# Performance work log

Measured on AMD Instinct MI355X. Metric: run time of the kernel, lower is better.

The kernel has to match this reference:

```python
import jax, jax.numpy as jnp
import numpy as np

FRACTION_BITS = 16
INTEGER_BITS = 16


def round_to_fixed(x):
    # floor-quantize to 2^-16 steps, clamp to signed 16-bit integer range
    delta = 2.0 ** (-FRACTION_BITS)
    bound = 2.0 ** (INTEGER_BITS - 1)
    return jnp.clip(jnp.floor(x / delta) * delta, -bound, bound - 1.0)


def setup_inputs() -> dict:
    key = jax.random.key(0)
    k1, k2, k3, k4 = jax.random.split(key, 4)
    N, IN_F, OUT_F = 4096, 4096, 4096
    inp = jax.random.normal(k1, (N, IN_F), dtype=jnp.float32)
    # reset_parameters: shift ~ U(-10,-1), sign ~ U(-1,0), bias ~ U(-b,b), b=1/sqrt(fan_in)
    shift = jax.random.uniform(k2, (OUT_F, IN_F), minval=-10.0, maxval=-1.0, dtype=jnp.float32)
    sign = jax.random.uniform(k3, (OUT_F, IN_F), minval=-1.0, maxval=0.0, dtype=jnp.float32)
    b = 1.0 / np.sqrt(IN_F)
    bias = jax.random.uniform(k4, (OUT_F,), minval=-b, maxval=b, dtype=jnp.float32)
    return {"input": inp, "shift": shift, "sign": sign, "bias": bias}


def reference(input, shift, sign, bias):
    # eager (non-kernel) path of LinearShiftFunction.forward
    q_in = round_to_fixed(input)
    q_bias = round_to_fixed(bias)
    s = jnp.clip(sign, -1.0, 1.0)
    v = jnp.exp2(jnp.round(shift)) * jnp.sign(s)  # [out_f, in_f] power-of-two weights
    out = q_in @ v.T + q_bias[None, :]
    return out
```

## Files before the change

### kernel.cpp

```cpp
#include <hip/hip_runtime.h>
#include <hip/hip_bf16.h>


#define BM 256
#define BN 256
#define BK 64

typedef __bf16 bf16_t;
typedef __attribute__((ext_vector_type(8))) __bf16 bf16x8;
typedef __attribute__((ext_vector_type(4))) __bf16 bf16x4;
typedef __attribute__((ext_vector_type(4))) float f32x4;

__device__ __forceinline__ float q16(float x) {
    float f = floorf(x * 65536.0f) * (1.0f / 65536.0f);
    return fminf(fmaxf(f, -32768.0f), 32767.0f);
}

__global__ void convert_kernel(const float* __restrict__ in,
                               const float* __restrict__ shift,
                               const float* __restrict__ sign_,
                               bf16_t* __restrict__ aq,
                               bf16_t* __restrict__ wq, int nvec) {
    int stride = gridDim.x * blockDim.x;
    for (int i = blockIdx.x * blockDim.x + threadIdx.x; i < nvec; i += stride) {
        float4 v = reinterpret_cast<const float4*>(in)[i];
        bf16x4 oa;
        oa[0] = (bf16_t)q16(v.x);
        oa[1] = (bf16_t)q16(v.y);
        oa[2] = (bf16_t)q16(v.z);
        oa[3] = (bf16_t)q16(v.w);
        reinterpret_cast<bf16x4*>(aq)[i] = oa;

        float4 sh = reinterpret_cast<const float4*>(shift)[i];
        float4 sg = reinterpret_cast<const float4*>(sign_)[i];
        float shs[4] = {sh.x, sh.y, sh.z, sh.w};
        float sgs[4] = {sg.x, sg.y, sg.z, sg.w};
        bf16x4 ow;
#pragma unroll
        for (int j = 0; j < 4; ++j) {
            float s = fminf(fmaxf(sgs[j], -1.0f), 1.0f);
            float sv = (s > 0.0f) ? 1.0f : ((s < 0.0f) ? -1.0f : 0.0f);
            ow[j] = (bf16_t)(exp2f(rintf(shs[j])) * sv);
        }
        reinterpret_cast<bf16x4*>(wq)[i] = ow;
    }
}


#define VMW(N) asm volatile("s_waitcnt vmcnt(" #N ")" ::: "memory")
#define BARF() do { __builtin_amdgcn_s_barrier(); asm volatile("" ::: "memory"); } while (0)

#define STAGE(LDSOFF, SRC) do {                                                          \
    const bf16_t* _s = (SRC);                                                            \
    bf16_t* _d = &lds[(LDSOFF)] + tid * 8;                                               \
    __builtin_amdgcn_global_load_lds((const __attribute__((address_space(1))) void*)_s,  \
                                     (__attribute__((address_space(3))) void*)_d,        \
                                     16, 0, 0);                                          \
    __builtin_amdgcn_global_load_lds(                                                    \
        (const __attribute__((address_space(1))) void*)(_s + (size_t)64 * K),            \
        (__attribute__((address_space(3))) void*)(_d + 4096), 16, 0, 0);                 \
} while (0)

#define READ_A(BUF, MH) do {                                                             \
    const bf16_t* _As = &lds[(BUF) * 32768 + wm * 8192];                                 \
    _Pragma("unroll") for (int m = 0; m < 4; ++m)                                        \
        _Pragma("unroll") for (int kk = 0; kk < 2; ++kk)                                 \
            af[m][kk] = *(const bf16x8*)&_As[((MH) * 64 + m * 16 + fr) * 64 +            \
                                             ((((kk << 2) | hi) ^ fr7) << 3)];           \
} while (0)

#define READ_B(BUF, NH, BF) do {                                                         \
    const bf16_t* _Bs = &lds[(BUF) * 32768 + 16384 + (wn >> 1) * 8192];                  \
    _Pragma("unroll") for (int n = 0; n < 2; ++n)                                        \
        _Pragma("unroll") for (int kk = 0; kk < 2; ++kk)                                 \
            BF[n][kk] = *(const bf16x8*)&_Bs[((wn & 1) * 64 + ((NH) * 2 + n) * 16 + fr)  \
                                                 * 64 +                                  \
                                             ((((kk << 2) | hi) ^ fr7) << 3)];           \
} while (0)

#define QUAD(MH, NH, BF) do {                                                            \
    _Pragma("unroll") for (int m = 0; m < 4; ++m)                                        \
        _Pragma("unroll") for (int n = 0; n < 2; ++n)                                    \
            _Pragma("unroll") for (int kk = 0; kk < 2; ++kk)                             \
                acc[(MH) * 4 + m][(NH) * 2 + n] =                                        \
                    __builtin_amdgcn_mfma_f32_16x16x32_bf16(                             \
                        af[m][kk], BF[n][kk], acc[(MH) * 4 + m][(NH) * 2 + n], 0, 0, 0); \
} while (0)

#define MFMA_PH(MH, NH, BF)                                                              \
    __builtin_amdgcn_s_setprio(1);                                                       \
    QUAD(MH, NH, BF);                                                                    \
    __builtin_amdgcn_s_setprio(0);

#define TILE(BUF, T, S0, S23, ENDW) do {                                                 \
                                                                            \
    if (S0) STAGE(((BUF) ^ 1) * 32768 + 1 * 8192, srcA1 + (size_t)((T) + 1) * 64);       \
    READ_A(BUF, 0);                                                                      \
    READ_B(BUF, 0, b0f);                                                                 \
    MFMA_PH(0, 0, b0f)                                                                   \
                                                                            \
    READ_B(BUF, 1, b1f);                                                                 \
    MFMA_PH(0, 1, b1f)                                                                   \
    BARF();                                                      \
                                                                            \
    if (S23) STAGE((BUF) * 32768 + 2 * 8192, srcB0 + (size_t)((T) + 2) * 64);            \
    READ_A(BUF, 1);                                                                      \
    MFMA_PH(1, 0, b0f)                                                                   \
                                          \
    if (S23) {                                                                           \
        STAGE((BUF) * 32768 + 0 * 8192, srcA0 + (size_t)((T) + 2) * 64);                 \
        STAGE((BUF) * 32768 + 3 * 8192, srcB1 + (size_t)((T) + 2) * 64);                 \
    }                                                                                    \
    MFMA_PH(1, 1, b1f)                                                                   \
    if ((ENDW) == 6) VMW(6);                                                             \
    else if ((ENDW) == 0) VMW(0);                                                        \
    BARF();                                                           \
} while (0)

__global__ __launch_bounds__(512, 2)
void gemm256_kernel(const bf16_t* __restrict__ A,
                    const bf16_t* __restrict__ B,
                    const float* __restrict__ bias,
                    float* __restrict__ C,
                    int M, int N, int K) {
    __shared__ bf16_t lds[65536];

    const int ntn = N / BN;
    const int nwg = gridDim.x;
    const int q = nwg >> 3, r = nwg & 7;
    const int xcd = blockIdx.x & 7, lid = blockIdx.x >> 3;
    const int swz = (xcd < r ? xcd * (q + 1) : r * (q + 1) + (xcd - r) * q) + lid;
    const int tile_m = (swz / ntn) * BM;
    const int tile_n = (swz % ntn) * BN;

    const int tid = threadIdx.x;
    const int lane = tid & 63;
    const int wid = tid >> 6;
    const int wm = wid >> 2;
    const int wn = wid & 3;
    const int fr = lane & 15;
    const int hi = lane >> 4;
    const int fr7 = fr & 7;

    const int colsrc_e = ((((tid & 7) * 16) ^ ((tid & 56) << 1)) >> 1);
    const bf16_t* srcA0 = A + (size_t)(tile_m + (tid >> 3)) * K + colsrc_e;
    const bf16_t* srcA1 = srcA0 + (size_t)128 * K;
    const bf16_t* srcB0 = B + (size_t)(tile_n + (tid >> 3)) * K + colsrc_e;
    const bf16_t* srcB1 = srcB0 + (size_t)128 * K;

    bf16x8 af[4][2], b0f[2][2], b1f[2][2];
    f32x4 acc[8][4] = {};

    STAGE(16384, srcB0);
    STAGE(0, srcA0);
    STAGE(24576, srcB1);
    STAGE(8192, srcA1);
    STAGE(32768 + 8192,  srcA1 + 64);
    STAGE(32768 + 16384, srcB0 + 64);
    STAGE(32768 + 0,     srcA0 + 64);
    STAGE(32768 + 24576, srcB1 + 64);
    VMW(6);
    BARF();

    const int npairs = K / 128;
    for (int i = 0; i < npairs - 1; ++i) {
        TILE(0, 2 * i, 1, 1, 6);
        TILE(1, 2 * i + 1, 1, 1, 6);
    }
    TILE(0, 2 * npairs - 2, 1, 0, 0);
    TILE(1, 2 * npairs - 1, 0, 0, -1);

    float qb[4];
#pragma unroll
    for (int ng = 0; ng < 4; ++ng)
        qb[ng] = q16(bias[tile_n + wn * 64 + ng * 16 + fr]);
#pragma unroll
    for (int mg = 0; mg < 8; ++mg) {
        const int grow0 = tile_m + wm * 128 + mg * 16 + hi * 4;
#pragma unroll
        for (int ng = 0; ng < 4; ++ng) {
            const int gcol = tile_n + wn * 64 + ng * 16 + fr;
#pragma unroll
            for (int rr = 0; rr < 4; ++rr)
                C[(size_t)(grow0 + rr) * N + gcol] = acc[mg][ng][rr] + qb[ng];
        }
    }
}

extern "C" void kernel_launch(void* const* d_in, const int* in_sizes, int n_in,
                              void* d_out, int out_size, void* d_ws, size_t ws_size,
                              hipStream_t stream) {
    const float* inp   = (const float*)d_in[0];
    const float* shift = (const float*)d_in[1];
    const float* sign_ = (const float*)d_in[2];
    const float* bias  = (const float*)d_in[3];
    float* out = (float*)d_out;

    const int OUT_F = in_sizes[3];
    const int IN_F  = in_sizes[1] / OUT_F;
    const int Mrows = in_sizes[0] / IN_F;

    bf16_t* Aq = (bf16_t*)d_ws;
    bf16_t* Wq = Aq + (size_t)Mrows * IN_F;

    const int nA = Mrows * IN_F;

    convert_kernel<<<2048, 256, 0, stream>>>(inp, shift, sign_, Aq, Wq, nA >> 2);

    dim3 grid((Mrows / BM) * (OUT_F / BN));
    gemm256_kernel<<<grid, 512, 0, stream>>>(Aq, Wq, bias, out,
                                             Mrows, OUT_F, IN_F);
}
```

Baseline: 158.2 us.

## Pre-pack weights in MFMA fragment order and load B directly from global

```diff
diff --git a/kernel.cpp b/kernel.cpp
--- a/kernel.cpp
+++ b/kernel.cpp
@@ -20,9 +20,11 @@
                                const float* __restrict__ shift,
                                const float* __restrict__ sign_,
                                bf16_t* __restrict__ aq,
-                               bf16_t* __restrict__ wq, int nvec) {
-    int stride = gridDim.x * blockDim.x;
-    for (int i = blockIdx.x * blockDim.x + threadIdx.x; i < nvec; i += stride) {
+                               bf16_t* __restrict__ wq,
+                               int nvecA, int nfragW, int K) {
+    const int stride = gridDim.x * blockDim.x;
+    const int t0 = blockIdx.x * blockDim.x + threadIdx.x;
+    for (int i = t0; i < nvecA; i += stride) {
         float4 v = reinterpret_cast<const float4*>(in)[i];
         bf16x4 oa;
         oa[0] = (bf16_t)q16(v.x);
@@ -30,19 +32,30 @@
         oa[2] = (bf16_t)q16(v.z);
         oa[3] = (bf16_t)q16(v.w);
         reinterpret_cast<bf16x4*>(aq)[i] = oa;
-
-        float4 sh = reinterpret_cast<const float4*>(shift)[i];
-        float4 sg = reinterpret_cast<const float4*>(sign_)[i];
-        float shs[4] = {sh.x, sh.y, sh.z, sh.w};
-        float sgs[4] = {sg.x, sg.y, sg.z, sg.w};
-        bf16x4 ow;
-#pragma unroll
-        for (int j = 0; j < 4; ++j) {
+    }
+    const int kbN = K >> 5;
+    for (int i = t0; i < nfragW; i += stride) {
+        const int lane = i & 63;
+        const int tmp = i >> 6;
+        const int kb = tmp % kbN;
+        const int g = tmp / kbN;
+        const int col = (g << 4) + (lane & 15);
+        const int k0 = kb * 32 + (lane >> 4) * 8;
+        const size_t off = (size_t)col * K + k0;
+        float4 sh0 = *reinterpret_cast<const float4*>(shift + off);
+        float4 sh1 = *reinterpret_cast<const float4*>(shift + off + 4);
+        float4 sg0 = *reinterpret_cast<const float4*>(sign_ + off);
+        float4 sg1 = *reinterpret_cast<const float4*>(sign_ + off + 4);
+        float shs[8] = {sh0.x, sh0.y, sh0.z, sh0.w, sh1.x, sh1.y, sh1.z, sh1.w};
+        float sgs[8] = {sg0.x, sg0.y, sg0.z, sg0.w, sg1.x, sg1.y, sg1.z, sg1.w};
+        bf16x8 ow;
+#pragma unroll
+        for (int j = 0; j < 8; ++j) {
             float s = fminf(fmaxf(sgs[j], -1.0f), 1.0f);
             float sv = (s > 0.0f) ? 1.0f : ((s < 0.0f) ? -1.0f : 0.0f);
             ow[j] = (bf16_t)(exp2f(rintf(shs[j])) * sv);
         }
-        reinterpret_cast<bf16x4*>(wq)[i] = ow;
+        reinterpret_cast<bf16x8*>(wq)[i] = ow;
     }
 }
 
@@ -62,20 +75,22 @@
 } while (0)
 
 #define READ_A(BUF, MH) do {                                                             \
-    const bf16_t* _As = &lds[(BUF) * 32768 + wm * 8192];                                 \
+    const bf16_t* _As = &lds[(BUF) * 16384 + wm * 8192];                                 \
     _Pragma("unroll") for (int m = 0; m < 4; ++m)                                        \
         _Pragma("unroll") for (int kk = 0; kk < 2; ++kk)                                 \
             af[m][kk] = *(const bf16x8*)&_As[((MH) * 64 + m * 16 + fr) * 64 +            \
                                              ((((kk << 2) | hi) ^ fr7) << 3)];           \
 } while (0)
 
-#define READ_B(BUF, NH, BF) do {                                                         \
-    const bf16_t* _Bs = &lds[(BUF) * 32768 + 16384 + (wn >> 1) * 8192];                  \
+#define LOADB0(T) do {                                                                   \
     _Pragma("unroll") for (int n = 0; n < 2; ++n)                                        \
         _Pragma("unroll") for (int kk = 0; kk < 2; ++kk)                                 \
-            BF[n][kk] = *(const bf16x8*)&_Bs[((wn & 1) * 64 + ((NH) * 2 + n) * 16 + fr)  \
-                                                 * 64 +                                  \
-                                             ((((kk << 2) | hi) ^ fr7) << 3)];           \
+            b0f[n][kk] = *(const bf16x8*)(gB[n] + ((size_t)(T) * 2 + kk) * 512);         \
+} while (0)
+#define LOADB1(T) do {                                                                   \
+    _Pragma("unroll") for (int n = 0; n < 2; ++n)                                        \
+        _Pragma("unroll") for (int kk = 0; kk < 2; ++kk)                                 \
+            b1f[n][kk] = *(const bf16x8*)(gB[n + 2] + ((size_t)(T) * 2 + kk) * 512);     \
 } while (0)
 
 #define QUAD(MH, NH, BF) do {                                                            \
@@ -92,38 +107,35 @@
     QUAD(MH, NH, BF);                                                                    \
     __builtin_amdgcn_s_setprio(0);
 
-#define TILE(BUF, T, S0, S23, ENDW) do {                                                 \
-                                                                            \
-    if (S0) STAGE(((BUF) ^ 1) * 32768 + 1 * 8192, srcA1 + (size_t)((T) + 1) * 64);       \
+#define TILE(BUF, T, S1, SB0, SA0, ENDW) do {                                            \
+                                                                            \
+    LOADB1(T);                                                                           \
+    if (S1) STAGE(((BUF) ^ 1) * 16384 + 8192, srcA1 + (size_t)((T) + 1) * 64);           \
     READ_A(BUF, 0);                                                                      \
-    READ_B(BUF, 0, b0f);                                                                 \
     MFMA_PH(0, 0, b0f)                                                                   \
                                                                             \
-    READ_B(BUF, 1, b1f);                                                                 \
     MFMA_PH(0, 1, b1f)                                                                   \
-    BARF();                                                      \
-                                                                            \
-    if (S23) STAGE((BUF) * 32768 + 2 * 8192, srcB0 + (size_t)((T) + 2) * 64);            \
+    BARF();                                                                              \
+                                                                            \
     READ_A(BUF, 1);                                                                      \
     MFMA_PH(1, 0, b0f)                                                                   \
-                                          \
-    if (S23) {                                                                           \
-        STAGE((BUF) * 32768 + 0 * 8192, srcA0 + (size_t)((T) + 2) * 64);                 \
-        STAGE((BUF) * 32768 + 3 * 8192, srcB1 + (size_t)((T) + 2) * 64);                 \
-    }                                                                                    \
+                                                                            \
+    if (SB0) LOADB0((T) + 1);                                                            \
+    if (SA0) STAGE((BUF) * 16384 + 0, srcA0 + (size_t)((T) + 2) * 64);                   \
     MFMA_PH(1, 1, b1f)                                                                   \
     if ((ENDW) == 6) VMW(6);                                                             \
+    else if ((ENDW) == 4) VMW(4);                                                        \
     else if ((ENDW) == 0) VMW(0);                                                        \
-    BARF();                                                           \
+    BARF();                                                                              \
 } while (0)
 
 __global__ __launch_bounds__(512, 2)
 void gemm256_kernel(const bf16_t* __restrict__ A,
-                    const bf16_t* __restrict__ B,
+                    const bf16_t* __restrict__ Wq,
                     const float* __restrict__ bias,
                     float* __restrict__ C,
                     int M, int N, int K) {
-    __shared__ bf16_t lds[65536];
+    __shared__ bf16_t lds[32768];
 
     const int ntn = N / BN;
     const int nwg = gridDim.x;
@@ -145,30 +157,30 @@
     const int colsrc_e = ((((tid & 7) * 16) ^ ((tid & 56) << 1)) >> 1);
     const bf16_t* srcA0 = A + (size_t)(tile_m + (tid >> 3)) * K + colsrc_e;
     const bf16_t* srcA1 = srcA0 + (size_t)128 * K;
-    const bf16_t* srcB0 = B + (size_t)(tile_n + (tid >> 3)) * K + colsrc_e;
-    const bf16_t* srcB1 = srcB0 + (size_t)128 * K;
+
+    const int kbN = K >> 5;
+    const bf16_t* gB[4];
+#pragma unroll
+    for (int rr = 0; rr < 4; ++rr)
+        gB[rr] = Wq + ((size_t)(tile_n / 16 + wn * 4 + rr) * kbN * 64 + lane) * 8;
 
     bf16x8 af[4][2], b0f[2][2], b1f[2][2];
     f32x4 acc[8][4] = {};
 
-    STAGE(16384, srcB0);
     STAGE(0, srcA0);
-    STAGE(24576, srcB1);
     STAGE(8192, srcA1);
-    STAGE(32768 + 8192,  srcA1 + 64);
-    STAGE(32768 + 16384, srcB0 + 64);
-    STAGE(32768 + 0,     srcA0 + 64);
-    STAGE(32768 + 24576, srcB1 + 64);
+    STAGE(16384 + 0, srcA0 + 64);
+    LOADB0(0);
     VMW(6);
     BARF();
 
     const int npairs = K / 128;
     for (int i = 0; i < npairs - 1; ++i) {
-        TILE(0, 2 * i, 1, 1, 6);
-        TILE(1, 2 * i + 1, 1, 1, 6);
-    }
-    TILE(0, 2 * npairs - 2, 1, 0, 0);
-    TILE(1, 2 * npairs - 1, 0, 0, -1);
+        TILE(0, 2 * i, 1, 1, 1, 6);
+        TILE(1, 2 * i + 1, 1, 1, 1, 6);
+    }
+    TILE(0, 2 * npairs - 2, 1, 1, 0, 4);
+    TILE(1, 2 * npairs - 1, 0, 0, 0, -1);
 
     float qb[4];
 #pragma unroll
@@ -204,8 +216,10 @@
     bf16_t* Wq = Aq + (size_t)Mrows * IN_F;
 
     const int nA = Mrows * IN_F;
-
-    convert_kernel<<<2048, 256, 0, stream>>>(inp, shift, sign_, Aq, Wq, nA >> 2);
+    const int nW = OUT_F * IN_F;
+
+    convert_kernel<<<2048, 256, 0, stream>>>(inp, shift, sign_, Aq, Wq,
+                                             nA >> 2, nW >> 3, IN_F);
 
     dim3 grid((Mrows / BM) * (OUT_F / BN));
     gemm256_kernel<<<grid, 512, 0, stream>>>(Aq, Wq, bias, out,
```

Measured after the change: 171.1 us. +8.2%, slower.
